# Performance work log

Measured on AMD Instinct MI355X. Metric: run time of the kernel, lower is better.

## Reference

```python
import jax, jax.numpy as jnp
import numpy as np

N_HEADS = 16

def _apply_rope(x, cos_pos, sin_pos):
    # x: [B,S,H,Dh]; cos_pos/sin_pos: [1,S,1,Dh//2]
    x1, x2 = jnp.split(x, 2, axis=-1)  # matches torch reshape (...,2,Dh//2) split
    x1r = x1 * cos_pos - x2 * sin_pos
    x2r = x2 * cos_pos + x1 * sin_pos
    return jnp.concatenate([x1r, x2r], axis=-1)

def setup_inputs() -> dict:
    key = jax.random.key(0)
    ks = jax.random.split(key, 8)
    B, S, D = 2, 2048, 1024
    Dh = D // N_HEADS
    hidden_states = jax.random.normal(ks[0], (B, S, D), dtype=jnp.float32)
    # rotary tables: cos/sin of theta; use realistic RoPE frequencies
    inv_freq = 1.0 / (10000.0 ** (jnp.arange(0, Dh, 2, dtype=jnp.float32) / Dh))  # [Dh//2]
    t = jnp.arange(S, dtype=jnp.float32)
    freqs = jnp.outer(t, inv_freq)  # [S, Dh//2]
    cos = jnp.cos(freqs)
    sin = jnp.sin(freqs)
    # additive causal mask [1,1,S,S]
    causal = jnp.tril(jnp.ones((S, S), dtype=bool))
    attention_mask = jnp.where(causal, 0.0, -1e9).astype(jnp.float32)[None, None]
    scale = 1.0 / np.sqrt(D)
    Wq = jax.random.normal(ks[1], (D, D), dtype=jnp.float32) * scale
    Wk = jax.random.normal(ks[2], (D, D), dtype=jnp.float32) * scale
    Wv = jax.random.normal(ks[3], (D, D), dtype=jnp.float32) * scale
    Wo = jax.random.normal(ks[4], (D, D), dtype=jnp.float32) * scale
    return {"hidden_states": hidden_states, "cos": cos, "sin": sin,
            "attention_mask": attention_mask, "Wq": Wq, "Wk": Wk, "Wv": Wv, "Wo": Wo}

def reference(hidden_states, cos, sin, attention_mask, Wq, Wk, Wv, Wo):
    B, S, D = hidden_states.shape
    H = N_HEADS
    Dh = D // H
    scaling = Dh ** -0.5
    q = (hidden_states @ Wq).reshape(B, S, H, Dh)
    k = (hidden_states @ Wk).reshape(B, S, H, Dh)
    v = (hidden_states @ Wv).reshape(B, S, H, Dh)
    cos_pos = cos[None, :, None, :]  # [1,S,1,Dh//2]
    sin_pos = sin[None, :, None, :]
    q = _apply_rope(q, cos_pos, sin_pos)
    k = _apply_rope(k, cos_pos, sin_pos)
    # eager attention: [B,H,S,S] scores
    scores = jnp.einsum('bihd,bjhd->bhij', q * scaling, k)
    scores = scores + attention_mask
    probs = jax.nn.softmax(scores, axis=-1)
    out = jnp.einsum('bhij,bjhd->bihd', probs, v).reshape(B, S, D)
    return out @ Wo
```

## Files before the change

### kernel.cpp

```cpp
#include <hip/hip_runtime.h>
#include <cstdint>
#include <cstddef>

using u16 = unsigned short;
using s16x8 = __attribute__((ext_vector_type(8))) short;
using f32x4 = __attribute__((ext_vector_type(4))) float;

#define GADDR(p) ((const __attribute__((address_space(1))) void*)(p))
#define LADDR(p) ((__attribute__((address_space(3))) void*)(p))

static constexpr int S_LEN = 2048;
static constexpr float L2E = 1.44269504088896f;

__device__ __forceinline__ u16 f2bf(float x) {
  union { float f; unsigned u; } v; v.f = x;
  return (u16)((v.u + 0x7FFFu + ((v.u >> 16) & 1u)) >> 16);
}
__device__ __forceinline__ unsigned pk_rn(float a, float b) {
  union { float f; unsigned u; } x, y; x.f = a; y.f = b;
  return ((x.u + 0x8000u) >> 16) | ((y.u + 0x8000u) & 0xFFFF0000u);
}
__device__ __forceinline__ float bf2f(u16 x) {
  union { unsigned u; float f; } v; v.u = (unsigned)x << 16;
  return v.f;
}

__device__ __constant__ unsigned char T_IT[48] = {
  31,31,30,30,29,28,15,14,
  29,28,27,27,26,26,25,24,13,12,
  25,24,23,23,22,22,21,20,11,10,
  21,20,19,19,18,18,17,16,9,8,
  17,16,7,6,
  5,4, 3,2, 1,0};
__device__ __constant__ unsigned char T_C0[48] = {
  0,1,0,1,0,0,0,0,
  1,1,0,1,0,1,0,0,0,0,
  1,1,0,1,0,1,0,0,0,0,
  1,1,0,1,0,1,0,0,0,0,
  1,1,0,0,
  0,0, 0,0, 0,0};

__global__ __launch_bounds__(256) void cast_x_k(const float* __restrict__ X,
                                                u16* __restrict__ Xb) {
  int i = (blockIdx.x * 256 + threadIdx.x) * 4;
  float4 v = *(const float4*)(X + i);
  u16* o = Xb + i;
  o[0] = f2bf(v.x); o[1] = f2bf(v.y); o[2] = f2bf(v.z); o[3] = f2bf(v.w);
}

__global__ __launch_bounds__(256) void transw_k(const float* __restrict__ Wq,
                                                const float* __restrict__ Wk,
                                                const float* __restrict__ Wv,
                                                const float* __restrict__ Wo,
                                                u16* __restrict__ WtAll) {
  const int z = blockIdx.z;
  const float* W = (z == 0) ? Wq : (z == 1) ? Wk : (z == 2) ? Wv : Wo;
  u16* Wt = WtAll + ((size_t)z << 20);
  const int k0 = blockIdx.x * 64, n0 = blockIdx.y * 64;
  const int tid = threadIdx.x;
  __shared__ float t[64][65];
  #pragma unroll
  for (int it = 0; it < 4; ++it) {
    int slot = it * 256 + tid;
    int r = slot >> 4, cq = slot & 15;
    float4 v = *(const float4*)&W[(size_t)(k0 + r) * 1024 + n0 + cq * 4];
    t[r][cq * 4 + 0] = v.x; t[r][cq * 4 + 1] = v.y;
    t[r][cq * 4 + 2] = v.z; t[r][cq * 4 + 3] = v.w;
  }
  __syncthreads();
  #pragma unroll
  for (int it = 0; it < 16; ++it) {
    int slot = it * 256 + tid;
    int rn = slot >> 6, ck = slot & 63;
    Wt[(size_t)(n0 + rn) * 1024 + k0 + ck] = f2bf(t[ck][rn]);
  }
}

__global__ __launch_bounds__(256, 2) void gemm_k(
    const u16* __restrict__ A, const u16* __restrict__ WtAll,
    const float* __restrict__ cosT, const float* __restrict__ sinT,
    u16* __restrict__ Qb, u16* __restrict__ Kb, u16* __restrict__ Vb,
    float* __restrict__ Of, int modeBase) {
  const int tid = threadIdx.x, lane = tid & 63, wv = tid >> 6;
  const int mode = modeBase + blockIdx.z;
  const u16* Wp = WtAll + ((size_t)mode << 20);
  const int m0 = blockIdx.x * 128, n0 = blockIdx.y * 128;
  const int wm = (wv >> 1) * 64, wn = (wv & 1) * 64;
  __shared__ __align__(16) u16 As[128 * 32];
  __shared__ __align__(16) u16 Bs[128 * 32];
  f32x4 acc[4][4];
  const f32x4 zf = {0.f, 0.f, 0.f, 0.f};
  #pragma unroll
  for (int i = 0; i < 4; ++i)
    #pragma unroll
    for (int j = 0; j < 4; ++j) acc[i][j] = zf;
  const int q = lane >> 4, l15 = lane & 15;

  for (int k0 = 0; k0 < 1024; k0 += 32) {
    __syncthreads();
    #pragma unroll
    for (int call = 0; call < 2; ++call) {
      int slot = call * 256 + tid;
      int row = slot >> 2, c = slot & 3;
      int sc = c ^ ((row >> 1) & 3);
      __builtin_amdgcn_global_load_lds(
          GADDR(A + (size_t)(m0 + row) * 1024 + k0 + sc * 8),
          LADDR(As + (size_t)(call * 256 + wv * 64) * 8), 16, 0, 0);
      __builtin_amdgcn_global_load_lds(
          GADDR(Wp + (size_t)(n0 + row) * 1024 + k0 + sc * 8),
          LADDR(Bs + (size_t)(call * 256 + wv * 64) * 8), 16, 0, 0);
    }
    __syncthreads();
    s16x8 af[4], bfr[4];
    #pragma unroll
    for (int mt = 0; mt < 4; ++mt) {
      int r = wm + mt * 16 + l15;
      af[mt] = *(const s16x8*)(As + r * 32 + ((q ^ ((r >> 1) & 3)) << 3));
    }
    #pragma unroll
    for (int nt = 0; nt < 4; ++nt) {
      int r = wn + nt * 16 + l15;
      bfr[nt] = *(const s16x8*)(Bs + r * 32 + ((q ^ ((r >> 1) & 3)) << 3));
    }
    #pragma unroll
    for (int mt = 0; mt < 4; ++mt)
      #pragma unroll
      for (int nt = 0; nt < 4; ++nt)
        acc[mt][nt] = __builtin_amdgcn_mfma_f32_16x16x32_bf16(af[mt], bfr[nt], acc[mt][nt], 0, 0, 0);
  }

  if (mode < 2) {
    u16* outP = (mode == 0) ? Qb : Kb;
    const float scl = (mode == 0) ? 0.125f * L2E : 1.0f;
    #pragma unroll
    for (int mt = 0; mt < 4; ++mt)
      #pragma unroll
      for (int rg = 0; rg < 4; ++rg) {
        int rowg = m0 + wm + mt * 16 + q * 4 + rg;
        int b = rowg >> 11, s = rowg & 2047;
        #pragma unroll
        for (int ntl = 0; ntl < 2; ++ntl) {
          int col = n0 + wn + ntl * 16 + l15;
          int h = col >> 6, dl = col & 31;
          float cc = cosT[s * 32 + dl], ss = sinT[s * 32 + dl];
          float xlo = acc[mt][ntl][rg];
          float xhi = acc[mt][ntl + 2][rg];
          size_t base = ((size_t)(b * 16 + h) * 2048 + s) * 64 + dl;
          outP[base]      = f2bf((xlo * cc - xhi * ss) * scl);
          outP[base + 32] = f2bf((xhi * cc + xlo * ss) * scl);
        }
      }
  } else if (mode == 2) {
    #pragma unroll
    for (int mt = 0; mt < 4; ++mt)
      #pragma unroll
      for (int rg = 0; rg < 4; ++rg) {
        int rowg = m0 + wm + mt * 16 + q * 4 + rg;
        int b = rowg >> 11, s = rowg & 2047;
        #pragma unroll
        for (int nt = 0; nt < 4; ++nt) {
          int col = n0 + wn + nt * 16 + l15;
          int h = col >> 6, d = col & 63;
          Vb[((size_t)(b * 16 + h) * 2048 + s) * 64 + d] = f2bf(acc[mt][nt][rg]);
        }
      }
  } else {
    #pragma unroll
    for (int mt = 0; mt < 4; ++mt)
      #pragma unroll
      for (int rg = 0; rg < 4; ++rg) {
        int rowg = m0 + wm + mt * 16 + q * 4 + rg;
        #pragma unroll
        for (int nt = 0; nt < 4; ++nt) {
          int col = n0 + wn + nt * 16 + l15;
          Of[(size_t)rowg * 1024 + col] = acc[mt][nt][rg];
        }
      }
  }
}

__global__ __launch_bounds__(256) void transv_k(const u16* __restrict__ Vb,
                                                u16* __restrict__ Vt) {
  const int tid = threadIdx.x;
  const int s0 = blockIdx.x * 64, bh = blockIdx.y;
  const u16* src = Vb + (size_t)bh * S_LEN * 64;
  u16* dst = Vt + (size_t)bh * 64 * S_LEN;
  __shared__ __align__(16) u16 t[64][80];
  #pragma unroll
  for (int it = 0; it < 2; ++it) {
    int slot = it * 256 + tid;
    int r = slot >> 3, c = slot & 7;
    s16x8 v = *(const s16x8*)(src + (size_t)(s0 + r) * 64 + c * 8);
    #pragma unroll
    for (int j = 0; j < 8; ++j) t[c * 8 + j][r] = (u16)v[j];
  }
  __syncthreads();
  #pragma unroll
  for (int it = 0; it < 2; ++it) {
    int slot = it * 256 + tid;
    int d = slot >> 3, c = slot & 7;
    s16x8 v = *(const s16x8*)(&t[d][c * 8]);
    *(s16x8*)(dst + (size_t)d * S_LEN + s0 + c * 8) = v;
  }
}

__global__ __launch_bounds__(256, 3) void flash_k(
    const u16* __restrict__ Qb, const u16* __restrict__ Kb,
    const u16* __restrict__ Vt, u16* __restrict__ Aout,
    char* __restrict__ Pscr, unsigned* __restrict__ qctr) {
  const int tid = threadIdx.x, lane = tid & 63, wv = tid >> 6;
  const int q = lane >> 4, l15 = lane & 15;
  __shared__ __align__(16) u16 Ks[128 * 64];
  __shared__ __align__(16) u16 Vs[64 * 128];
  __shared__ __align__(16) u16 Ps[4][16 * 128];
  __shared__ unsigned s_c;
  u16* Pw = Ps[wv];
  const f32x4 zf = {0.f, 0.f, 0.f, 0.f};

  for (;;) {
    if (tid == 0) s_c = atomicAdd(qctr, 1u);
    __syncthreads();
    const unsigned c = s_c;
    if (c >= 1536u) break;
    const int bh = (int)(c & 31u), local = (int)(c >> 5);
    const int it = T_IT[local], c0 = T_C0[local];
    const int len = (it >> 1) + 1, mid = (len + 1) >> 1;
    const int jt0 = c0 ? mid : 0;
    const int jtE = (it >= 16) ? (c0 ? len : mid) : len;
    const int i0 = it * 64;
    const int iw = i0 + wv * 16 + l15;
    const u16* Qh = Qb + (size_t)bh * S_LEN * 64;
    const u16* Kh = Kb + (size_t)bh * S_LEN * 64;
    const u16* Vh = Vt + (size_t)bh * 64 * S_LEN;

    s16x8 bq[2];
    #pragma unroll
    for (int ks = 0; ks < 2; ++ks)
      bq[ks] = *(const s16x8*)(Qh + (size_t)iw * 64 + ks * 32 + q * 8);

    f32x4 O[4];
    float mst = -1e30f, lst = 0.f;
    #pragma unroll
    for (int i = 0; i < 4; ++i) O[i] = zf;

    for (int jt = jt0; jt < jtE; ++jt) {
      const int j0 = jt * 128;
      __syncthreads();
      #pragma unroll
      for (int cc = 0; cc < 4; ++cc) {
        const int wc = cc * 4 + wv;
        {
          int jr = wc * 8 + (lane >> 3);
          int u = (lane & 7) ^ (jr & 7);
          __builtin_amdgcn_global_load_lds(
              GADDR(Kh + (size_t)(j0 + jr) * 64 + u * 8),
              LADDR(Ks + wc * 512), 16, 0, 0);
        }
        {
          int d = wc * 4 + (lane >> 4);
          int uv = (lane & 15) ^ (d & 15);
          __builtin_amdgcn_global_load_lds(
              GADDR(Vh + (size_t)d * S_LEN + j0 + uv * 8),
              LADDR(Vs + wc * 512), 16, 0, 0);
        }
      }
      __syncthreads();

      f32x4 sf[8];
      #pragma unroll
      for (int j = 0; j < 8; ++j) sf[j] = zf;
      #pragma unroll
      for (int ks = 0; ks < 2; ++ks)
        #pragma unroll
        for (int mt = 0; mt < 8; ++mt) {
          int jr = mt * 16 + l15;
          int u = ((ks * 4 + q) ^ (jr & 7));
          s16x8 ak = *(const s16x8*)(Ks + jr * 64 + u * 8);
          sf[mt] = __builtin_amdgcn_mfma_f32_16x16x32_bf16(ak, bq[ks], sf[mt], 0, 0, 0);
        }

      if (jt == len - 1) {
        #pragma unroll
        for (int mt = 0; mt < 8; ++mt)
          #pragma unroll
          for (int rg = 0; rg < 4; ++rg) {
            int j = j0 + mt * 16 + q * 4 + rg;
            if (j > iw) sf[mt][rg] = -1e30f;
          }
      }

      float mx = sf[0][0];
      #pragma unroll
      for (int mt = 0; mt < 8; ++mt)
        #pragma unroll
        for (int rg = 0; rg < 4; ++rg) mx = fmaxf(mx, sf[mt][rg]);
      mx = fmaxf(mx, __shfl_xor(mx, 16, 64));
      mx = fmaxf(mx, __shfl_xor(mx, 32, 64));
      float mn = fmaxf(mst, mx);
      float al = exp2f(mst - mn);
      mst = mn;
      float sum = 0.f;
      #pragma unroll
      for (int mt = 0; mt < 8; ++mt) {
        float p0 = exp2f(sf[mt][0] - mn), p1 = exp2f(sf[mt][1] - mn);
        float p2 = exp2f(sf[mt][2] - mn), p3 = exp2f(sf[mt][3] - mn);
        sum += (p0 + p1) + (p2 + p3);
        uint2 pk; pk.x = pk_rn(p0, p1); pk.y = pk_rn(p2, p3);
        int cj = (mt * 4 + q) ^ l15;
        *(uint2*)(Pw + l15 * 128 + cj * 4) = pk;
      }
      sum += __shfl_xor(sum, 16, 64);
      sum += __shfl_xor(sum, 32, 64);
      lst = al * lst + sum;
      #pragma unroll
      for (int ntd = 0; ntd < 4; ++ntd)
        #pragma unroll
        for (int rg = 0; rg < 4; ++rg) O[ntd][rg] *= al;

      asm volatile("s_waitcnt lgkmcnt(0)" ::: "memory");

      s16x8 bp[4];
      #pragma unroll
      for (int ks = 0; ks < 4; ++ks) {
        int u0 = ks * 8 + q * 2;
        union { s16x8 v; uint2 d[2]; } f;
        f.d[0] = *(const uint2*)(Pw + l15 * 128 + ((u0) ^ l15) * 4);
        f.d[1] = *(const uint2*)(Pw + l15 * 128 + ((u0 + 1) ^ l15) * 4);
        bp[ks] = f.v;
      }
      #pragma unroll
      for (int ks = 0; ks < 4; ++ks)
        #pragma unroll
        for (int ntd = 0; ntd < 4; ++ntd) {
          int d = ntd * 16 + l15;
          int uv = (ks * 4 + q) ^ l15;
          s16x8 av = *(const s16x8*)(Vs + d * 128 + uv * 8);
          O[ntd] = __builtin_amdgcn_mfma_f32_16x16x32_bf16(av, bp[ks], O[ntd], 0, 0, 0);
        }
    }

    if (it < 16) {
      const float inv = 1.0f / lst;
      const int b = bh >> 4, h = bh & 15;
      u16* dst = Aout + ((size_t)(b * 2048 + iw)) * 1024 + h * 64;
      #pragma unroll
      for (int ntd = 0; ntd < 4; ++ntd) {
        uint2 pk;
        pk.x = pk_rn(O[ntd][0] * inv, O[ntd][1] * inv);
        pk.y = pk_rn(O[ntd][2] * inv, O[ntd][3] * inv);
        *(uint2*)(dst + ntd * 16 + q * 4) = pk;
      }
    } else {
      const int slot = (bh * 16 + (it - 16)) * 2 + c0;
      char* pb = Pscr + (size_t)slot * 8704;
      float* Pm = (float*)pb;
      u16* Po = (u16*)(pb + 512);
      const int il = wv * 16 + l15;
      if (q == 0) { Pm[il] = mst; Pm[64 + il] = lst; }
      #pragma unroll
      for (int ntd = 0; ntd < 4; ++ntd) {
        uint2 pk;
        pk.x = pk_rn(O[ntd][0], O[ntd][1]);
        pk.y = pk_rn(O[ntd][2], O[ntd][3]);
        *(uint2*)(Po + il * 64 + ntd * 16 + q * 4) = pk;
      }
    }
    __syncthreads();
  }
}

__global__ __launch_bounds__(256) void combine_k(const char* __restrict__ Pscr,
                                                 u16* __restrict__ Aout) {
  const int blk = blockIdx.x;
  const int bh = blk >> 4, itm = blk & 15;
  const char* b0 = Pscr + (size_t)((bh * 16 + itm) * 2 + 0) * 8704;
  const char* b1 = Pscr + (size_t)((bh * 16 + itm) * 2 + 1) * 8704;
  const int t = threadIdx.x;
  const int r = t >> 2, dseg = (t & 3) * 16;
  const float m0 = ((const float*)b0)[r], l0 = ((const float*)b0)[64 + r];
  const float m1 = ((const float*)b1)[r], l1 = ((const float*)b1)[64 + r];
  const float M = fmaxf(m0, m1);
  const float w0 = exp2f(m0 - M), w1 = exp2f(m1 - M);
  const float inv = 1.0f / (w0 * l0 + w1 * l1);
  const u16* O0 = (const u16*)(b0 + 512) + r * 64 + dseg;
  const u16* O1 = (const u16*)(b1 + 512) + r * 64 + dseg;
  u16 outv[16];
  #pragma unroll
  for (int v8 = 0; v8 < 2; ++v8) {
    s16x8 a = *(const s16x8*)(O0 + v8 * 8);
    s16x8 bb = *(const s16x8*)(O1 + v8 * 8);
    #pragma unroll
    for (int j = 0; j < 8; ++j)
      outv[v8 * 8 + j] = f2bf((w0 * bf2f((u16)a[j]) + w1 * bf2f((u16)bb[j])) * inv);
  }
  const int b = bh >> 4, h = bh & 15;
  const int s = (itm + 16) * 64 + r;
  u16* dst = Aout + ((size_t)(b * 2048 + s)) * 1024 + h * 64 + dseg;
  *(uint4*)dst = *(const uint4*)outv;
  *(uint4*)(dst + 8) = *(const uint4*)(outv + 8);
}

extern "C" void kernel_launch(void* const* d_in, const int* in_sizes, int n_in,
                              void* d_out, int out_size, void* d_ws, size_t ws_size,
                              hipStream_t stream) {
  const float* X    = (const float*)d_in[0];
  const float* cosT = (const float*)d_in[1];
  const float* sinT = (const float*)d_in[2];
  const float* Wq = (const float*)d_in[4];
  const float* Wk = (const float*)d_in[5];
  const float* Wv = (const float*)d_in[6];
  const float* Wo = (const float*)d_in[7];
  float* Of = (float*)d_out;

  u16* ws  = (u16*)d_ws;
  u16* Xb  = ws;
  u16* Wt  = ws + (4u << 20);
  u16* Qb  = ws + (8u << 20);
  u16* Kb  = ws + (12u << 20);
  u16* Vb  = ws + (16u << 20);
  u16* Vtb = ws + (20u << 20);
  unsigned* qctr = (unsigned*)Vb;
  char* Pscr = (char*)d_out;

  cast_x_k<<<4096, 256, 0, stream>>>(X, Xb);
  transw_k<<<dim3(16, 16, 4), 256, 0, stream>>>(Wq, Wk, Wv, Wo, Wt);
  gemm_k<<<dim3(32, 8, 3), 256, 0, stream>>>(Xb, Wt, cosT, sinT, Qb, Kb, Vb, nullptr, 0);
  transv_k<<<dim3(32, 32), 256, 0, stream>>>(Vb, Vtb);
  hipMemsetAsync(qctr, 0, 4, stream);
  flash_k<<<768, 256, 0, stream>>>(Qb, Kb, Vtb, Xb, Pscr, qctr);
  combine_k<<<512, 256, 0, stream>>>(Pscr, Xb);
  gemm_k<<<dim3(32, 8, 1), 256, 0, stream>>>(Xb, Wt, cosT, sinT, nullptr, nullptr, nullptr, Of, 3);
}
```

Baseline: 217.8 us.

## Fuse prep kernels, write V transposed from GEMM, statically schedule flash work

Merges the X cast and weight transpose into one launch. The V-projection GEMM epilogue now writes V directly in transposed [bh][d][s] layout with packed 4-element stores, which removes the separate transpose kernel. The flash kernel replaces its atomic work-queue counter and memset with a static pairing: each block takes item blockIdx and item 1535-blockIdx to balance causal work. The cost is losing dynamic load balancing, and the transposed V stores are strided in global memory.

```diff
diff --git a/kernel.cpp b/kernel.cpp
--- a/kernel.cpp
+++ b/kernel.cpp
@@ -40,24 +40,26 @@
   1,1,0,0,
   0,0, 0,0, 0,0};
 
-__global__ __launch_bounds__(256) void cast_x_k(const float* __restrict__ X,
-                                                u16* __restrict__ Xb) {
-  int i = (blockIdx.x * 256 + threadIdx.x) * 4;
-  float4 v = *(const float4*)(X + i);
-  u16* o = Xb + i;
-  o[0] = f2bf(v.x); o[1] = f2bf(v.y); o[2] = f2bf(v.z); o[3] = f2bf(v.w);
-}
-
-__global__ __launch_bounds__(256) void transw_k(const float* __restrict__ Wq,
-                                                const float* __restrict__ Wk,
-                                                const float* __restrict__ Wv,
-                                                const float* __restrict__ Wo,
-                                                u16* __restrict__ WtAll) {
-  const int z = blockIdx.z;
+__global__ __launch_bounds__(256) void prep_k(const float* __restrict__ X,
+                                              u16* __restrict__ Xb,
+                                              const float* __restrict__ Wq,
+                                              const float* __restrict__ Wk,
+                                              const float* __restrict__ Wv,
+                                              const float* __restrict__ Wo,
+                                              u16* __restrict__ WtAll) {
+  const int bid = blockIdx.x, tid = threadIdx.x;
+  if (bid < 4096) {
+    int i = (bid * 256 + tid) * 4;
+    float4 v = *(const float4*)(X + i);
+    u16* o = Xb + i;
+    o[0] = f2bf(v.x); o[1] = f2bf(v.y); o[2] = f2bf(v.z); o[3] = f2bf(v.w);
+    return;
+  }
+  const int r4 = bid - 4096;
+  const int z = r4 >> 8, rem = r4 & 255;
   const float* W = (z == 0) ? Wq : (z == 1) ? Wk : (z == 2) ? Wv : Wo;
   u16* Wt = WtAll + ((size_t)z << 20);
-  const int k0 = blockIdx.x * 64, n0 = blockIdx.y * 64;
-  const int tid = threadIdx.x;
+  const int k0 = (rem >> 4) * 64, n0 = (rem & 15) * 64;
   __shared__ float t[64][65];
   #pragma unroll
   for (int it = 0; it < 4; ++it) {
@@ -79,7 +81,7 @@
 __global__ __launch_bounds__(256, 2) void gemm_k(
     const u16* __restrict__ A, const u16* __restrict__ WtAll,
     const float* __restrict__ cosT, const float* __restrict__ sinT,
-    u16* __restrict__ Qb, u16* __restrict__ Kb, u16* __restrict__ Vb,
+    u16* __restrict__ Qb, u16* __restrict__ Kb, u16* __restrict__ Vt,
     float* __restrict__ Of, int modeBase) {
   const int tid = threadIdx.x, lane = tid & 63, wv = tid >> 6;
   const int mode = modeBase + blockIdx.z;
@@ -152,18 +154,19 @@
       }
   } else if (mode == 2) {
     #pragma unroll
-    for (int mt = 0; mt < 4; ++mt)
-      #pragma unroll
-      for (int rg = 0; rg < 4; ++rg) {
-        int rowg = m0 + wm + mt * 16 + q * 4 + rg;
-        int b = rowg >> 11, s = rowg & 2047;
-        #pragma unroll
-        for (int nt = 0; nt < 4; ++nt) {
-          int col = n0 + wn + nt * 16 + l15;
-          int h = col >> 6, d = col & 63;
-          Vb[((size_t)(b * 16 + h) * 2048 + s) * 64 + d] = f2bf(acc[mt][nt][rg]);
-        }
-      }
+    for (int mt = 0; mt < 4; ++mt) {
+      int rowg = m0 + wm + mt * 16 + q * 4;
+      int b = rowg >> 11, s = rowg & 2047;
+      #pragma unroll
+      for (int nt = 0; nt < 4; ++nt) {
+        int col = n0 + wn + nt * 16 + l15;
+        int h = col >> 6, d = col & 63;
+        uint2 pk;
+        pk.x = pk_rn(acc[mt][nt][0], acc[mt][nt][1]);
+        pk.y = pk_rn(acc[mt][nt][2], acc[mt][nt][3]);
+        *(uint2*)(Vt + ((size_t)((b * 16 + h) * 64 + d) * 2048 + s)) = pk;
+      }
+    }
   } else {
     #pragma unroll
     for (int mt = 0; mt < 4; ++mt)
@@ -179,49 +182,21 @@
   }
 }
 
-__global__ __launch_bounds__(256) void transv_k(const u16* __restrict__ Vb,
-                                                u16* __restrict__ Vt) {
-  const int tid = threadIdx.x;
-  const int s0 = blockIdx.x * 64, bh = blockIdx.y;
-  const u16* src = Vb + (size_t)bh * S_LEN * 64;
-  u16* dst = Vt + (size_t)bh * 64 * S_LEN;
-  __shared__ __align__(16) u16 t[64][80];
-  #pragma unroll
-  for (int it = 0; it < 2; ++it) {
-    int slot = it * 256 + tid;
-    int r = slot >> 3, c = slot & 7;
-    s16x8 v = *(const s16x8*)(src + (size_t)(s0 + r) * 64 + c * 8);
-    #pragma unroll
-    for (int j = 0; j < 8; ++j) t[c * 8 + j][r] = (u16)v[j];
-  }
-  __syncthreads();
-  #pragma unroll
-  for (int it = 0; it < 2; ++it) {
-    int slot = it * 256 + tid;
-    int d = slot >> 3, c = slot & 7;
-    s16x8 v = *(const s16x8*)(&t[d][c * 8]);
-    *(s16x8*)(dst + (size_t)d * S_LEN + s0 + c * 8) = v;
-  }
-}
-
 __global__ __launch_bounds__(256, 3) void flash_k(
     const u16* __restrict__ Qb, const u16* __restrict__ Kb,
     const u16* __restrict__ Vt, u16* __restrict__ Aout,
-    char* __restrict__ Pscr, unsigned* __restrict__ qctr) {
+    char* __restrict__ Pscr) {
   const int tid = threadIdx.x, lane = tid & 63, wv = tid >> 6;
   const int q = lane >> 4, l15 = lane & 15;
   __shared__ __align__(16) u16 Ks[128 * 64];
   __shared__ __align__(16) u16 Vs[64 * 128];
   __shared__ __align__(16) u16 Ps[4][16 * 128];
-  __shared__ unsigned s_c;
   u16* Pw = Ps[wv];
   const f32x4 zf = {0.f, 0.f, 0.f, 0.f};
 
-  for (;;) {
-    if (tid == 0) s_c = atomicAdd(qctr, 1u);
-    __syncthreads();
-    const unsigned c = s_c;
-    if (c >= 1536u) break;
+  #pragma unroll 1
+  for (int half = 0; half < 2; ++half) {
+    const unsigned c = half ? (1535u - blockIdx.x) : blockIdx.x;
     const int bh = (int)(c & 31u), local = (int)(c >> 5);
     const int it = T_IT[local], c0 = T_C0[local];
     const int len = (it >> 1) + 1, mid = (len + 1) >> 1;
@@ -365,7 +340,6 @@
         *(uint2*)(Po + il * 64 + ntd * 16 + q * 4) = pk;
       }
     }
-    __syncthreads();
   }
 }
 
@@ -417,17 +391,12 @@
   u16* Wt  = ws + (4u << 20);
   u16* Qb  = ws + (8u << 20);
   u16* Kb  = ws + (12u << 20);
-  u16* Vb  = ws + (16u << 20);
   u16* Vtb = ws + (20u << 20);
-  unsigned* qctr = (unsigned*)Vb;
   char* Pscr = (char*)d_out;
 
-  cast_x_k<<<4096, 256, 0, stream>>>(X, Xb);
-  transw_k<<<dim3(16, 16, 4), 256, 0, stream>>>(Wq, Wk, Wv, Wo, Wt);
-  gemm_k<<<dim3(32, 8, 3), 256, 0, stream>>>(Xb, Wt, cosT, sinT, Qb, Kb, Vb, nullptr, 0);
-  transv_k<<<dim3(32, 32), 256, 0, stream>>>(Vb, Vtb);
-  hipMemsetAsync(qctr, 0, 4, stream);
-  flash_k<<<768, 256, 0, stream>>>(Qb, Kb, Vtb, Xb, Pscr, qctr);
+  prep_k<<<5120, 256, 0, stream>>>(X, Xb, Wq, Wk, Wv, Wo, Wt);
+  gemm_k<<<dim3(32, 8, 3), 256, 0, stream>>>(Xb, Wt, cosT, sinT, Qb, Kb, Vtb, nullptr, 0);
+  flash_k<<<768, 256, 0, stream>>>(Qb, Kb, Vtb, Xb, Pscr);
   combine_k<<<512, 256, 0, stream>>>(Pscr, Xb);
   gemm_k<<<dim3(32, 8, 1), 256, 0, stream>>>(Xb, Wt, cosT, sinT, nullptr, nullptr, nullptr, Of, 3);
 }
```

After: 201.5 us. 1.08x faster.
